# Kernel optimization log

Measured on AMD Instinct MI355X. Metric: run time of the kernel, lower is better.

Reference implementation:

```python
import math
import jax, jax.numpy as jnp
import numpy as np

HEADS = 9
EMBED = 32
TEMPERATURE = 3000.0

def _conv1x1(x, W, b):
    # x: [B,C,H,W], W: [O,C], b: [O]  (1x1 conv == channel matmul)
    return jnp.einsum('bchw,oc->bohw', x, W) + b[None, :, None, None]

def setup_inputs() -> dict:
    key = jax.random.key(0)
    ks = jax.random.split(key, 14)
    B, H, W = 2, 64, 64
    h2, w2 = 32, 32
    hd = HEADS * EMBED  # 288
    s = 0.1
    return {
        'second_frame': jax.random.normal(ks[0], (B, 3, H, W), jnp.float32),
        'first_frame_aligned': jax.random.normal(ks[1], (B, 3, H, W), jnp.float32),
        'second_frame_feat': jax.random.normal(ks[2], (B, 4, h2, w2), jnp.float32),
        'first_frame_feat_aligned': jax.random.normal(ks[3], (B, 4, h2, w2), jnp.float32),
        'Wq': jax.random.normal(ks[4], (hd, 3), jnp.float32) * s,
        'bq': jax.random.normal(ks[5], (hd,), jnp.float32) * s,
        'Wk': jax.random.normal(ks[6], (hd, 3), jnp.float32) * s,
        'bk': jax.random.normal(ks[7], (hd,), jnp.float32) * s,
        'Wv': jax.random.normal(ks[8], (hd, 4), jnp.float32) * s,
        'bv': jax.random.normal(ks[9], (hd,), jnp.float32) * s,
        'Wp': jax.random.normal(ks[10], (4, hd), jnp.float32) * s,
        'bp': jax.random.normal(ks[11], (4,), jnp.float32) * s,
        'Wt': jax.random.normal(ks[12], (1, EMBED), jnp.float32) * s,
        'bt': jax.random.normal(ks[13], (1,), jnp.float32) * s,
    }

def reference(second_frame, first_frame_aligned, second_frame_feat,
              first_frame_feat_aligned, Wq, bq, Wk, bk, Wv, bv, Wp, bp, Wt, bt):
    B, _, H, W = second_frame.shape
    HW = H * W
    # bilinear upsample of aligned features to (H, W); half-pixel centers == align_corners=False
    feat_up = jax.image.resize(first_frame_feat_aligned,
                               (B, first_frame_feat_aligned.shape[1], H, W),
                               method='linear', antialias=False)
    Q = _conv1x1(second_frame, Wq, bq).reshape(B, HEADS, EMBED, HW)
    K = _conv1x1(first_frame_aligned, Wk, bk).reshape(B, HEADS, EMBED, HW)
    V = _conv1x1(feat_up, Wv, bv).reshape(B, HEADS, EMBED, HW)
    Qn = jnp.transpose(Q, (0, 1, 3, 2))                      # [B,h,HW,d]
    sim = jnp.einsum('bhnd,bhdm->bhnm', Qn, K) / math.sqrt(EMBED)  # [B,h,HW,HW]
    # learned per-query threshold from Q
    t = jnp.einsum('bhnd,od->bhno', Qn, Wt) + bt             # [B,h,HW,1]
    attn = jax.nn.relu((sim - t) / TEMPERATURE)              # no row normalization
    out = jnp.einsum('bhnm,bhdm->bhnd', attn, V)             # [B,h,HW,d]
    out = jnp.transpose(out, (0, 1, 3, 2)).reshape(B, HEADS * EMBED, H, W)
    out_feat = _conv1x1(out, Wp, bp)                         # [B,4,H,W]
    h2, w2 = second_frame_feat.shape[-2:]
    out_feat_down = jax.image.resize(out_feat, (B, out_feat.shape[1], h2, w2),
                                     method='linear', antialias=False)
    final_feat = second_frame_feat + out_feat_down
    return final_feat, out_feat_down
```

## Files before the change

kernel.cpp:

```cpp
#include <hip/hip_runtime.h>
#include <hip/hip_bf16.h>
#include <cstddef>

#define NHEADS 9
#define D 32
#define SQ 4096
#define ZSPLIT 8
#define MBLK (SQ / ZSPLIT)
#define CHUNKS (MBLK / 64)

typedef __attribute__((ext_vector_type(8))) short bf16x8;
typedef __attribute__((ext_vector_type(4))) float f32x4;

__device__ __forceinline__ unsigned int f2bf(float f) {
    unsigned int u = __float_as_uint(f);
    u += 0x7fffu + ((u >> 16) & 1u);
    return u >> 16;
}

__device__ __forceinline__ unsigned int trunc_pk(float lo, float hi) {
    return __builtin_amdgcn_perm(__float_as_uint(hi), __float_as_uint(lo),
                                 0x07060302u);
}

__device__ __forceinline__ bf16x8 relu_pack8(f32x4 s1, f32x4 s2) {
    union { unsigned int u[4]; bf16x8 v; } P;
    P.u[0] = trunc_pk(s1[0], s1[1]);
    P.u[1] = trunc_pk(s1[2], s1[3]);
    P.u[2] = trunc_pk(s2[0], s2[1]);
    P.u[3] = trunc_pk(s2[2], s2[3]);
    const bf16x8 z = {0, 0, 0, 0, 0, 0, 0, 0};
    return __builtin_elementwise_max(P.v, z);
}

__device__ __forceinline__ void gload_lds16(const unsigned short* g,
                                            unsigned short* l) {
    __builtin_amdgcn_global_load_lds(
        (const __attribute__((address_space(1))) unsigned int*)g,
        (__attribute__((address_space(3))) unsigned int*)l, 16, 0, 0);
}

__global__ __launch_bounds__(256) void prep_kernel(
    const float* __restrict__ x2, const float* __restrict__ x1,
    const float* __restrict__ feat1,
    const float* __restrict__ Wq, const float* __restrict__ bq,
    const float* __restrict__ Wk, const float* __restrict__ bk,
    const float* __restrict__ Wv, const float* __restrict__ bv,
    const float* __restrict__ Wt, const float* __restrict__ bt,
    unsigned short* __restrict__ Qb, unsigned short* __restrict__ Kb,
    unsigned short* __restrict__ Vt, float* __restrict__ tbuf)
{
    __shared__ unsigned short Vls[32 * 66];

    const int tid = threadIdx.x;
    int idx = blockIdx.x * blockDim.x + tid;
    int g  = idx & 3;
    int nl = tid >> 2;
    int n  = (idx >> 2) & (SQ - 1);
    int bh = idx >> 14;
    int h  = bh % NHEADS;
    int b  = bh / NHEADS;

    float xs0 = x2[((size_t)b * 3 + 0) * SQ + n];
    float xs1 = x2[((size_t)b * 3 + 1) * SQ + n];
    float xs2 = x2[((size_t)b * 3 + 2) * SQ + n];
    float ys0 = x1[((size_t)b * 3 + 0) * SQ + n];
    float ys1 = x1[((size_t)b * 3 + 1) * SQ + n];
    float ys2 = x1[((size_t)b * 3 + 2) * SQ + n];

    int yy = n >> 6, xx = n & 63;
    int jy = yy >> 1, jx = xx >> 1;
    int j0, j1, i0, i1; float wy0, wy1, wx0, wx1;
    if (yy & 1) { j0 = jy; j1 = (jy < 31) ? jy + 1 : 31; wy0 = 0.75f; wy1 = 0.25f; }
    else        { j0 = (jy > 0) ? jy - 1 : 0; j1 = jy;   wy0 = 0.25f; wy1 = 0.75f; }
    if (xx & 1) { i0 = jx; i1 = (jx < 31) ? jx + 1 : 31; wx0 = 0.75f; wx1 = 0.25f; }
    else        { i0 = (jx > 0) ? jx - 1 : 0; i1 = jx;   wx0 = 0.25f; wx1 = 0.75f; }

    float fu[4];
#pragma unroll
    for (int c = 0; c < 4; ++c) {
        const float* f = feat1 + ((size_t)b * 4 + c) * 1024;
        fu[c] = wy0 * (wx0 * f[j0 * 32 + i0] + wx1 * f[j0 * 32 + i1]) +
                wy1 * (wx0 * f[j1 * 32 + i0] + wx1 * f[j1 * 32 + i1]);
    }

    const int d0 = g * 8;
    unsigned int qp[4], kp[4];
    float tpart = 0.0f;
#pragma unroll
    for (int j = 0; j < 8; ++j) {
        int d = d0 + j, hd = h * D + d;
        float q = bq[hd] + Wq[hd * 3] * xs0 + Wq[hd * 3 + 1] * xs1 + Wq[hd * 3 + 2] * xs2;
        float k = bk[hd] + Wk[hd * 3] * ys0 + Wk[hd * 3 + 1] * ys1 + Wk[hd * 3 + 2] * ys2;
        float v = bv[hd] + Wv[hd * 4] * fu[0] + Wv[hd * 4 + 1] * fu[1] +
                  Wv[hd * 4 + 2] * fu[2] + Wv[hd * 4 + 3] * fu[3];
        tpart += q * Wt[d];
        unsigned int qb_ = f2bf(q), kb_ = f2bf(k);
        if (j & 1) { qp[j >> 1] |= qb_ << 16; kp[j >> 1] |= kb_ << 16; }
        else       { qp[j >> 1]  = qb_;       kp[j >> 1]  = kb_; }
        Vls[d * 66 + nl] = (unsigned short)f2bf(v);
    }
    tpart += __shfl_xor(tpart, 1);
    tpart += __shfl_xor(tpart, 2);
    if (g == 0) tbuf[(size_t)bh * SQ + n] = tpart + bt[0];

    *(uint4*)(Qb + ((size_t)bh * SQ + n) * D + d0) =
        make_uint4(qp[0], qp[1], qp[2], qp[3]);

    {
        int nl_  = n & 63;
        int slot = (nl_ & 32) + 4 * ((nl_ >> 3) & 3) + (nl_ & 3) + ((nl_ & 4) << 2);
        size_t kaddr = ((size_t)bh * SQ + (n & ~63) + slot) * D + d0;
        *(uint4*)(Kb + kaddr) = make_uint4(kp[0], kp[1], kp[2], kp[3]);
    }

    __syncthreads();
    {
        int r   = tid >> 3;
        int c4  = tid & 7;
        int blk = blockIdx.x & 63;
        unsigned int w0 = *(const unsigned int*)&Vls[r * 66 + c4 * 8];
        unsigned int w1 = *(const unsigned int*)&Vls[r * 66 + c4 * 8 + 2];
        unsigned int w2 = *(const unsigned int*)&Vls[r * 66 + c4 * 8 + 4];
        unsigned int w3 = *(const unsigned int*)&Vls[r * 66 + c4 * 8 + 6];
        size_t dst = ((size_t)bh * 128 + blk * 2 + (c4 >> 2)) * 1024
                   + (r >> 4) * 512 + (c4 & 3) * 128 + (r & 15) * 8;
        *(uint4*)(Vt + dst) = make_uint4(w0, w1, w2, w3);
    }
}

#define STEP_COMPUTE(K1, K2, VL, VH)                                           \
    {                                                                          \
        f32x4 sA1 = __builtin_amdgcn_mfma_f32_16x16x32_bf16(K1, qfA, ciA, 0, 0, 0);\
        f32x4 sA2 = __builtin_amdgcn_mfma_f32_16x16x32_bf16(K2, qfA, ciA, 0, 0, 0);\
        f32x4 sB1 = __builtin_amdgcn_mfma_f32_16x16x32_bf16(K1, qfB, ciB, 0, 0, 0);\
        f32x4 sB2 = __builtin_amdgcn_mfma_f32_16x16x32_bf16(K2, qfB, ciB, 0, 0, 0);\
        f32x4 sC1 = __builtin_amdgcn_mfma_f32_16x16x32_bf16(K1, qfC, ciC, 0, 0, 0);\
        f32x4 sC2 = __builtin_amdgcn_mfma_f32_16x16x32_bf16(K2, qfC, ciC, 0, 0, 0);\
        f32x4 sD1 = __builtin_amdgcn_mfma_f32_16x16x32_bf16(K1, qfD, ciD, 0, 0, 0);\
        f32x4 sD2 = __builtin_amdgcn_mfma_f32_16x16x32_bf16(K2, qfD, ciD, 0, 0, 0);\
        bf16x8 pA = relu_pack8(sA1, sA2);                                      \
        bf16x8 pB = relu_pack8(sB1, sB2);                                      \
        bf16x8 pC = relu_pack8(sC1, sC2);                                      \
        bf16x8 pD = relu_pack8(sD1, sD2);                                      \
        accAl = __builtin_amdgcn_mfma_f32_16x16x32_bf16(VL, pA, accAl, 0, 0, 0);\
        accAh = __builtin_amdgcn_mfma_f32_16x16x32_bf16(VH, pA, accAh, 0, 0, 0);\
        accBl = __builtin_amdgcn_mfma_f32_16x16x32_bf16(VL, pB, accBl, 0, 0, 0);\
        accBh = __builtin_amdgcn_mfma_f32_16x16x32_bf16(VH, pB, accBh, 0, 0, 0);\
        accCl = __builtin_amdgcn_mfma_f32_16x16x32_bf16(VL, pC, accCl, 0, 0, 0);\
        accCh = __builtin_amdgcn_mfma_f32_16x16x32_bf16(VH, pC, accCh, 0, 0, 0);\
        accDl = __builtin_amdgcn_mfma_f32_16x16x32_bf16(VL, pD, accDl, 0, 0, 0);\
        accDh = __builtin_amdgcn_mfma_f32_16x16x32_bf16(VH, pD, accDh, 0, 0, 0);\
    }

__global__ __launch_bounds__(512, 4) void attn_kernel(
    const unsigned short* __restrict__ Qb,
    const unsigned short* __restrict__ Kb,
    const unsigned short* __restrict__ Vt,
    const float* __restrict__ tbuf,
    const float* __restrict__ Wp,
    float* __restrict__ ofp)
{
    __shared__ __align__(16) unsigned short Kls[3][2048];
    __shared__ __align__(16) unsigned short Vls3[3][2048];

    const int lin  = blockIdx.x;
    const int xcd  = lin & 7;
    const int q8   = lin >> 3;
    const int xblk = q8 & 7;
    const int gl   = q8 >> 3;
    const int grp  = xcd * 18 + gl;
    const int bh   = grp >> 3;
    const int zz   = grp & 7;
    const int h    = bh % NHEADS;
    const int n0   = xblk * 512;
    const int mc0  = zz * MBLK;
    const int tid  = threadIdx.x;
    const int wave = tid >> 6;
    const int lane = tid & 63;
    const int l15  = lane & 15;
    const int quad = lane >> 4;

    const int nw = n0 + wave * 64;

    const unsigned short* qbase = Qb + ((size_t)bh * SQ + nw + l15) * D + quad * 8;
    bf16x8 qfA = *(const bf16x8*)(qbase);
    bf16x8 qfB = *(const bf16x8*)(qbase + 16 * D);
    bf16x8 qfC = *(const bf16x8*)(qbase + 32 * D);
    bf16x8 qfD = *(const bf16x8*)(qbase + 48 * D);

    const float SQRT32 = 5.656854249492381f;
    const float* tb = tbuf + (size_t)bh * SQ + nw + l15;
    float TA = tb[0]  * SQRT32;
    float TB = tb[16] * SQRT32;
    float TC = tb[32] * SQRT32;
    float TD = tb[48] * SQRT32;
    const f32x4 ciA = {-TA, -TA, -TA, -TA};
    const f32x4 ciB = {-TB, -TB, -TB, -TB};
    const f32x4 ciC = {-TC, -TC, -TC, -TC};
    const f32x4 ciD = {-TD, -TD, -TD, -TD};

    const int qtr = wave & 3;
    const unsigned short* Sg =
        (wave < 4) ? (Kb + ((size_t)bh * SQ + mc0) * D + qtr * 512 + lane * 8)
                   : (Vt + ((size_t)bh * 128 + (mc0 >> 5)) * 1024 + qtr * 512 + lane * 8);
    const int sdoff = qtr * 512;

    const int koff = l15 * 32 + quad * 8;
    const int voff = lane * 8;

#define ISSUE(C, S)                                                            \
    gload_lds16(Sg + (size_t)(C) * 2048,                                       \
                ((wave < 4) ? &Kls[S][sdoff] : &Vls3[S][sdoff]));

#define CCHUNK(S)                                                              \
    {                                                                          \
        const unsigned short* Kp = &Kls[S][0];                                 \
        const unsigned short* Vp = &Vls3[S][0];                                \
        bf16x8 k1 = *(const bf16x8*)(Kp + koff);                               \
        bf16x8 k2 = *(const bf16x8*)(Kp + 512 + koff);                         \
        bf16x8 vl = *(const bf16x8*)(Vp + voff);                               \
        bf16x8 vh = *(const bf16x8*)(Vp + 512 + voff);                         \
        __builtin_amdgcn_s_setprio(1);                                         \
        STEP_COMPUTE(k1, k2, vl, vh);                                          \
        __builtin_amdgcn_s_setprio(0);                                         \
        k1 = *(const bf16x8*)(Kp + 1024 + koff);                               \
        k2 = *(const bf16x8*)(Kp + 1536 + koff);                               \
        vl = *(const bf16x8*)(Vp + 1024 + voff);                               \
        vh = *(const bf16x8*)(Vp + 1536 + voff);                               \
        __builtin_amdgcn_s_setprio(1);                                         \
        STEP_COMPUTE(k1, k2, vl, vh);                                          \
        __builtin_amdgcn_s_setprio(0);                                         \
    }

    f32x4 accAl = {0.f,0.f,0.f,0.f}, accAh = {0.f,0.f,0.f,0.f};
    f32x4 accBl = {0.f,0.f,0.f,0.f}, accBh = {0.f,0.f,0.f,0.f};
    f32x4 accCl = {0.f,0.f,0.f,0.f}, accCh = {0.f,0.f,0.f,0.f};
    f32x4 accDl = {0.f,0.f,0.f,0.f}, accDh = {0.f,0.f,0.f,0.f};

    ISSUE(0, 0);
    ISSUE(1, 1);

#pragma unroll
    for (int c = 0; c < CHUNKS; ++c) {
        asm volatile("s_waitcnt vmcnt(1)" ::: "memory");
        __builtin_amdgcn_s_barrier();
        {
            const int nc = (c + 2 < CHUNKS) ? c + 2 : CHUNKS - 1;
            ISSUE(nc, (c + 2) % 3);
        }
        CCHUNK(c % 3);
    }
    asm volatile("s_waitcnt vmcnt(0)" ::: "memory");

    const float s1 = 5.892556509887896e-05f;
    const float* wph = Wp + h * D + quad * 4;
    float* obase = ofp + ((size_t)(bh * 8 + zz) * 4) * SQ + nw + l15;
#pragma unroll
    for (int o = 0; o < 4; ++o) {
        float cA = 0.f, cB = 0.f, cC = 0.f, cD = 0.f;
#pragma unroll
        for (int r = 0; r < 4; ++r) {
            float wlo = wph[o * 288 + r], whi = wph[o * 288 + 16 + r];
            cA += accAl[r] * wlo + accAh[r] * whi;
            cB += accBl[r] * wlo + accBh[r] * whi;
            cC += accCl[r] * wlo + accCh[r] * whi;
            cD += accDl[r] * wlo + accDh[r] * whi;
        }
        cA += __shfl_xor(cA, 16); cA += __shfl_xor(cA, 32);
        cB += __shfl_xor(cB, 16); cB += __shfl_xor(cB, 32);
        cC += __shfl_xor(cC, 16); cC += __shfl_xor(cC, 32);
        cD += __shfl_xor(cD, 16); cD += __shfl_xor(cD, 32);
        if (quad == 0) {
            float* ob = obase + (size_t)o * SQ;
            ob[0]  = cA * s1;
            ob[16] = cB * s1;
            ob[32] = cC * s1;
            ob[48] = cD * s1;
        }
    }
}

__global__ __launch_bounds__(256) void final_kernel(
    const float* __restrict__ ofp,
    const float* __restrict__ sff,
    const float* __restrict__ bp,
    float* __restrict__ dout)
{
    int t = blockIdx.x * 256 + threadIdx.x;
    int out = t >> 3;
    int s   = t & 7;
    int i  = out & 31;
    int jj = (out >> 5) & 31;
    int bo = out >> 10;
    int o  = bo & 3;
    int b  = bo >> 2;
    int nbase = (jj * 2) * 64 + i * 2;

    float acc = 0.0f;
#pragma unroll
    for (int h = 0; h < NHEADS; ++h) {
        const float* src = ofp +
            ((size_t)(((b * NHEADS + h) * 8 + s) * 4 + o)) * SQ + nbase;
        acc += src[0] + src[1] + src[64] + src[65];
    }
    acc += __shfl_xor(acc, 1);
    acc += __shfl_xor(acc, 2);
    acc += __shfl_xor(acc, 4);
    if (s == 0) {
        float dval = 0.25f * acc + bp[o];
        dout[out]        = sff[out] + dval;
        dout[8192 + out] = dval;
    }
}

extern "C" void kernel_launch(void* const* d_in, const int* in_sizes, int n_in,
                              void* d_out, int out_size, void* d_ws, size_t ws_size,
                              hipStream_t stream)
{
    const float* second_frame = (const float*)d_in[0];
    const float* first_frame  = (const float*)d_in[1];
    const float* sff          = (const float*)d_in[2];
    const float* ffa          = (const float*)d_in[3];
    const float* Wq = (const float*)d_in[4];
    const float* bq = (const float*)d_in[5];
    const float* Wk = (const float*)d_in[6];
    const float* bk = (const float*)d_in[7];
    const float* Wv = (const float*)d_in[8];
    const float* bv = (const float*)d_in[9];
    const float* Wp = (const float*)d_in[10];
    const float* bp = (const float*)d_in[11];
    const float* Wt = (const float*)d_in[12];
    const float* bt = (const float*)d_in[13];
    float* out = (float*)d_out;

    char* ws = (char*)d_ws;
    const size_t QKV = (size_t)2 * NHEADS * SQ * D * sizeof(unsigned short);
    unsigned short* Qb = (unsigned short*)ws;
    unsigned short* Kb = (unsigned short*)(ws + QKV);
    unsigned short* Vt = (unsigned short*)(ws + 2 * QKV);
    float* tbuf = (float*)(ws + 3 * QKV);
    float* ofp  = (float*)(ws + 3 * QKV + (size_t)2 * NHEADS * SQ * sizeof(float));

    prep_kernel<<<1152, 256, 0, stream>>>(second_frame, first_frame, ffa,
                                          Wq, bq, Wk, bk, Wv, bv, Wt, bt,
                                          Qb, Kb, Vt, tbuf);
    attn_kernel<<<8 * 18 * ZSPLIT, 512, 0, stream>>>(Qb, Kb, Vt, tbuf, Wp, ofp);
    final_kernel<<<256, 256, 0, stream>>>(ofp, sff, bp, out);
}
```

Baseline: 134.8 us.

## Double attention chunk size per barrier and make prep compute full head rows per thread

The attention kernel now loads two 64-key chunks per pipeline stage, with two async global-to-LDS loads per thread and a wait count of 2. This halves the number of barriers and waitcnt stalls per block but doubles the LDS footprint to 48KB. The prep kernel is reorganised so each thread computes all 32 dims for one pixel, which removes the shuffles and writes full 64-byte Q/K rows, at the cost of more registers and half as many threads.

```diff
diff --git a/kernel.cpp b/kernel.cpp
--- a/kernel.cpp
+++ b/kernel.cpp
@@ -8,6 +8,7 @@
 #define ZSPLIT 8
 #define MBLK (SQ / ZSPLIT)
 #define CHUNKS (MBLK / 64)
+#define PERIODS (CHUNKS / 2)
 
 typedef __attribute__((ext_vector_type(8))) short bf16x8;
 typedef __attribute__((ext_vector_type(4))) float f32x4;
@@ -40,7 +41,7 @@
         (__attribute__((address_space(3))) unsigned int*)l, 16, 0, 0);
 }
 
-__global__ __launch_bounds__(256) void prep_kernel(
+__global__ __launch_bounds__(128) void prep_kernel(
     const float* __restrict__ x2, const float* __restrict__ x1,
     const float* __restrict__ feat1,
     const float* __restrict__ Wq, const float* __restrict__ bq,
@@ -50,16 +51,15 @@
     unsigned short* __restrict__ Qb, unsigned short* __restrict__ Kb,
     unsigned short* __restrict__ Vt, float* __restrict__ tbuf)
 {
-    __shared__ unsigned short Vls[32 * 66];
+    __shared__ unsigned short Vls[32 * 136];
 
     const int tid = threadIdx.x;
-    int idx = blockIdx.x * blockDim.x + tid;
-    int g  = idx & 3;
-    int nl = tid >> 2;
-    int n  = (idx >> 2) & (SQ - 1);
-    int bh = idx >> 14;
-    int h  = bh % NHEADS;
-    int b  = bh / NHEADS;
+    const int blk = blockIdx.x;
+    const int bh  = blk >> 5;
+    const int nr  = blk & 31;
+    const int n   = nr * 128 + tid;
+    const int h   = bh % NHEADS;
+    const int b   = bh / NHEADS;
 
     float xs0 = x2[((size_t)b * 3 + 0) * SQ + n];
     float xs1 = x2[((size_t)b * 3 + 1) * SQ + n];
@@ -84,48 +84,54 @@
                 wy1 * (wx0 * f[j1 * 32 + i0] + wx1 * f[j1 * 32 + i1]);
     }
 
-    const int d0 = g * 8;
-    unsigned int qp[4], kp[4];
+    unsigned int qp[16], kp[16];
     float tpart = 0.0f;
 #pragma unroll
-    for (int j = 0; j < 8; ++j) {
-        int d = d0 + j, hd = h * D + d;
+    for (int d = 0; d < 32; ++d) {
+        int hd = h * D + d;
         float q = bq[hd] + Wq[hd * 3] * xs0 + Wq[hd * 3 + 1] * xs1 + Wq[hd * 3 + 2] * xs2;
         float k = bk[hd] + Wk[hd * 3] * ys0 + Wk[hd * 3 + 1] * ys1 + Wk[hd * 3 + 2] * ys2;
         float v = bv[hd] + Wv[hd * 4] * fu[0] + Wv[hd * 4 + 1] * fu[1] +
                   Wv[hd * 4 + 2] * fu[2] + Wv[hd * 4 + 3] * fu[3];
         tpart += q * Wt[d];
         unsigned int qb_ = f2bf(q), kb_ = f2bf(k);
-        if (j & 1) { qp[j >> 1] |= qb_ << 16; kp[j >> 1] |= kb_ << 16; }
-        else       { qp[j >> 1]  = qb_;       kp[j >> 1]  = kb_; }
-        Vls[d * 66 + nl] = (unsigned short)f2bf(v);
-    }
-    tpart += __shfl_xor(tpart, 1);
-    tpart += __shfl_xor(tpart, 2);
-    if (g == 0) tbuf[(size_t)bh * SQ + n] = tpart + bt[0];
-
-    *(uint4*)(Qb + ((size_t)bh * SQ + n) * D + d0) =
-        make_uint4(qp[0], qp[1], qp[2], qp[3]);
-
+        if (d & 1) { qp[d >> 1] |= qb_ << 16; kp[d >> 1] |= kb_ << 16; }
+        else       { qp[d >> 1]  = qb_;       kp[d >> 1]  = kb_; }
+        Vls[d * 136 + tid] = (unsigned short)f2bf(v);
+    }
+    tbuf[(size_t)bh * SQ + n] = tpart + bt[0];
+
+    {
+        size_t qa = ((size_t)bh * SQ + n) * D;
+#pragma unroll
+        for (int r4 = 0; r4 < 4; ++r4)
+            *(uint4*)(Qb + qa + r4 * 8) =
+                make_uint4(qp[r4 * 4], qp[r4 * 4 + 1], qp[r4 * 4 + 2], qp[r4 * 4 + 3]);
+    }
     {
         int nl_  = n & 63;
         int slot = (nl_ & 32) + 4 * ((nl_ >> 3) & 3) + (nl_ & 3) + ((nl_ & 4) << 2);
-        size_t kaddr = ((size_t)bh * SQ + (n & ~63) + slot) * D + d0;
-        *(uint4*)(Kb + kaddr) = make_uint4(kp[0], kp[1], kp[2], kp[3]);
+        size_t ka = ((size_t)bh * SQ + (n & ~63) + slot) * D;
+#pragma unroll
+        for (int r4 = 0; r4 < 4; ++r4)
+            *(uint4*)(Kb + ka + r4 * 8) =
+                make_uint4(kp[r4 * 4], kp[r4 * 4 + 1], kp[r4 * 4 + 2], kp[r4 * 4 + 3]);
     }
 
     __syncthreads();
-    {
-        int r   = tid >> 3;
-        int c4  = tid & 7;
-        int blk = blockIdx.x & 63;
-        unsigned int w0 = *(const unsigned int*)&Vls[r * 66 + c4 * 8];
-        unsigned int w1 = *(const unsigned int*)&Vls[r * 66 + c4 * 8 + 2];
-        unsigned int w2 = *(const unsigned int*)&Vls[r * 66 + c4 * 8 + 4];
-        unsigned int w3 = *(const unsigned int*)&Vls[r * 66 + c4 * 8 + 6];
-        size_t dst = ((size_t)bh * 128 + blk * 2 + (c4 >> 2)) * 1024
-                   + (r >> 4) * 512 + (c4 & 3) * 128 + (r & 15) * 8;
-        *(uint4*)(Vt + dst) = make_uint4(w0, w1, w2, w3);
+#pragma unroll
+    for (int rep = 0; rep < 4; ++rep) {
+        int li  = rep * 128 + tid;
+        int r   = li >> 4;
+        int oct = li & 15;
+        const unsigned short* src = &Vls[r * 136 + oct * 8];
+        uint4 w = make_uint4(*(const unsigned int*)src,
+                             *(const unsigned int*)(src + 2),
+                             *(const unsigned int*)(src + 4),
+                             *(const unsigned int*)(src + 6));
+        size_t dst = ((size_t)bh * 128 + nr * 4 + (oct >> 2)) * 1024
+                   + (r >> 4) * 512 + (oct & 3) * 128 + (r & 15) * 8;
+        *(uint4*)(Vt + dst) = w;
     }
 }
 
@@ -161,8 +167,8 @@
     const float* __restrict__ Wp,
     float* __restrict__ ofp)
 {
-    __shared__ __align__(16) unsigned short Kls[3][2048];
-    __shared__ __align__(16) unsigned short Vls3[3][2048];
+    __shared__ __align__(16) unsigned short Kls[3][4096];
+    __shared__ __align__(16) unsigned short Vls3[3][4096];
 
     const int lin  = blockIdx.x;
     const int xcd  = lin & 7;
@@ -209,14 +215,16 @@
     const int koff = l15 * 32 + quad * 8;
     const int voff = lane * 8;
 
-#define ISSUE(C, S)                                                            \
-    gload_lds16(Sg + (size_t)(C) * 2048,                                       \
-                ((wave < 4) ? &Kls[S][sdoff] : &Vls3[S][sdoff]));
-
-#define CCHUNK(S)                                                              \
+#define ISSUE2(P, S)                                                           \
+    gload_lds16(Sg + (size_t)(P) * 4096,                                       \
+                ((wave < 4) ? &Kls[S][sdoff] : &Vls3[S][sdoff]));              \
+    gload_lds16(Sg + (size_t)(P) * 4096 + 2048,                                \
+                ((wave < 4) ? &Kls[S][2048 + sdoff] : &Vls3[S][2048 + sdoff]));
+
+#define CCHUNK(S, OFF)                                                         \
     {                                                                          \
-        const unsigned short* Kp = &Kls[S][0];                                 \
-        const unsigned short* Vp = &Vls3[S][0];                                \
+        const unsigned short* Kp = &Kls[S][OFF];                               \
+        const unsigned short* Vp = &Vls3[S][OFF];                              \
         bf16x8 k1 = *(const bf16x8*)(Kp + koff);                               \
         bf16x8 k2 = *(const bf16x8*)(Kp + 512 + koff);                         \
         bf16x8 vl = *(const bf16x8*)(Vp + voff);                               \
@@ -238,18 +246,19 @@
     f32x4 accCl = {0.f,0.f,0.f,0.f}, accCh = {0.f,0.f,0.f,0.f};
     f32x4 accDl = {0.f,0.f,0.f,0.f}, accDh = {0.f,0.f,0.f,0.f};
 
-    ISSUE(0, 0);
-    ISSUE(1, 1);
-
-#pragma unroll
-    for (int c = 0; c < CHUNKS; ++c) {
-        asm volatile("s_waitcnt vmcnt(1)" ::: "memory");
+    ISSUE2(0, 0);
+    ISSUE2(1, 1);
+
+#pragma unroll
+    for (int p = 0; p < PERIODS; ++p) {
+        asm volatile("s_waitcnt vmcnt(2)" ::: "memory");
         __builtin_amdgcn_s_barrier();
         {
-            const int nc = (c + 2 < CHUNKS) ? c + 2 : CHUNKS - 1;
-            ISSUE(nc, (c + 2) % 3);
+            const int np = (p + 2 < PERIODS) ? p + 2 : PERIODS - 1;
+            ISSUE2(np, (p + 2) % 3);
         }
-        CCHUNK(c % 3);
+        CCHUNK(p % 3, 0);
+        CCHUNK(p % 3, 2048);
     }
     asm volatile("s_waitcnt vmcnt(0)" ::: "memory");
 
@@ -342,9 +351,9 @@
     float* tbuf = (float*)(ws + 3 * QKV);
     float* ofp  = (float*)(ws + 3 * QKV + (size_t)2 * NHEADS * SQ * sizeof(float));
 
-    prep_kernel<<<1152, 256, 0, stream>>>(second_frame, first_frame, ffa,
-                                          Wq, bq, Wk, bk, Wv, bv, Wt, bt,
-                                          Qb, Kb, Vt, tbuf);
+    prep_kernel<<<576, 128, 0, stream>>>(second_frame, first_frame, ffa,
+                                         Wq, bq, Wk, bk, Wv, bv, Wt, bt,
+                                         Qb, Kb, Vt, tbuf);
     attn_kernel<<<8 * 18 * ZSPLIT, 512, 0, stream>>>(Qb, Kb, Vt, tbuf, Wp, ofp);
     final_kernel<<<256, 256, 0, stream>>>(ofp, sff, bp, out);
 }
```

Measured after the change: 136.5 us. No clear change (+1.3%).
